# Performance work log

Hardware: AMD Instinct MI355X
Metric: run time of the kernel (lower is better)

## Reference

```python
import jax, jax.numpy as jnp
import numpy as np

NUM_HEADS = 16
HEAD_DIM = 128
NUM_KV_HEADS = 8
NUM_KV_GROUPS = 2
HIDDEN = 2048
SCALE = 0.5  # hardcoded in the original SDPA call


def _fixed_sincos_pos(E, H):
    # matches ReusedProjReconstructor._fixed_sincos_pos (H even here)
    half = H // 2
    freq = jnp.exp(-jnp.log(jnp.float32(10000.0)) * jnp.arange(half, dtype=jnp.float32) / half)
    pos = jnp.arange(E, dtype=jnp.float32)[:, None]
    ang = pos * freq[None, :]
    return jnp.concatenate([jnp.sin(ang), jnp.cos(ang)], axis=1)  # [E, H]


def setup_inputs() -> dict:
    key = jax.random.key(0)
    ks = jax.random.split(key, 8)
    B, M, H = 4, 2048, HIDDEN
    kv_dim = NUM_KV_HEADS * HEAD_DIM
    s = 0.02
    return {
        "mem_act": jax.random.normal(ks[0], (B, M, H), jnp.float32),
        "Wq": jax.random.normal(ks[1], (H, H), jnp.float32) * s,
        "bq": jax.random.normal(ks[2], (H,), jnp.float32) * s,
        "Wk": jax.random.normal(ks[3], (kv_dim, H), jnp.float32) * s,
        "bk": jax.random.normal(ks[4], (kv_dim,), jnp.float32) * s,
        "Wv": jax.random.normal(ks[5], (kv_dim, H), jnp.float32) * s,
        "bv": jax.random.normal(ks[6], (kv_dim,), jnp.float32) * s,
        "Wo": jax.random.normal(ks[7], (H, H), jnp.float32) * s,
        "E": 2048,
    }


def reference(mem_act, Wq, bq, Wk, bk, Wv, bv, Wo, E):
    B, M, H = mem_act.shape
    # positional query hidden, shared across batch (q_ln is Identity)
    q_hidden = _fixed_sincos_pos(E, H).astype(mem_act.dtype)  # [E, H]
    q = (q_hidden @ Wq.T + bq).reshape(E, NUM_HEADS, HEAD_DIM)          # [E, nh, hd]
    k = (mem_act @ Wk.T + bk).reshape(B, M, NUM_KV_HEADS, HEAD_DIM)     # [B, M, nkv, hd]
    v = (mem_act @ Wv.T + bv).reshape(B, M, NUM_KV_HEADS, HEAD_DIM)
    # GQA: repeat kv heads (repeat_interleave over head dim)
    k = jnp.repeat(k, NUM_KV_GROUPS, axis=2)  # [B, M, nh, hd]
    v = jnp.repeat(v, NUM_KV_GROUPS, axis=2)
    # non-causal SDPA with scale=0.5, query broadcast over batch
    scores = jnp.einsum("ehd,bmhd->bhem", q, k) * SCALE  # [B, nh, E, M]
    attn = jax.nn.softmax(scores, axis=-1)
    out = jnp.einsum("bhem,bmhd->behd", attn, v).reshape(B, E, H)
    pred = out @ Wo.T  # o_proj (no bias, Qwen2 style)
    return pred
```

## Files before the change

### kernel.cpp

```cpp
#include <hip/hip_runtime.h>
#include <hip/hip_bf16.h>

typedef __attribute__((ext_vector_type(8))) short short8;
typedef __attribute__((ext_vector_type(4))) float f32x4;
typedef __attribute__((ext_vector_type(16))) float f32x16;
typedef unsigned short ushort_t;

__device__ __forceinline__ unsigned short f2bf(float x) {
    unsigned int u = __builtin_bit_cast(unsigned int, x);
    unsigned int r = (u + 0x7fffu + ((u >> 16) & 1u)) >> 16;
    return (unsigned short)r;
}

__device__ __forceinline__ void gload_lds16(const ushort_t* g, ushort_t* l) {
    __builtin_amdgcn_global_load_lds(
        (const __attribute__((address_space(1))) void*)g,
        (__attribute__((address_space(3))) void*)l, 16, 0, 0);
}

#define MFMA16(A, B, C) __builtin_amdgcn_mfma_f32_16x16x32_bf16((A), (B), (C), 0, 0, 0)
#define MFMA32(A, B, C) __builtin_amdgcn_mfma_f32_32x32x16_bf16((A), (B), (C), 0, 0, 0)

__global__ __launch_bounds__(256) void cvt_f32_bf16(const float* __restrict__ in,
                                                    ushort_t* __restrict__ out, int n) {
    int i = (blockIdx.x * 256 + threadIdx.x) << 3;
    if (i >= n) return;
    const float4* p = (const float4*)(in + i);
    float4 a = p[0], b = p[1];
    short8 o;
    o[0] = (short)f2bf(a.x); o[1] = (short)f2bf(a.y);
    o[2] = (short)f2bf(a.z); o[3] = (short)f2bf(a.w);
    o[4] = (short)f2bf(b.x); o[5] = (short)f2bf(b.y);
    o[6] = (short)f2bf(b.z); o[7] = (short)f2bf(b.w);
    *(short8*)(out + i) = o;
}

__global__ __launch_bounds__(256) void fill_qh(ushort_t* __restrict__ qh) {
    int idx = blockIdx.x * 256 + threadIdx.x;
    int e = idx >> 10, i = idx & 1023;
    float freq = __expf(-9.2103403719761836f * (float)i * (1.0f / 1024.0f));
    float ang = (float)e * freq;
    qh[(size_t)e * 2048 + i]        = f2bf(sinf(ang));
    qh[(size_t)e * 2048 + 1024 + i] = f2bf(cosf(ang));
}

__global__ __launch_bounds__(256) void gemm_q(const ushort_t* __restrict__ A,
                                              const ushort_t* __restrict__ Bw,
                                              const float* __restrict__ bias,
                                              ushort_t* __restrict__ Cout,
                                              int M, int N, int K) {
    __shared__ ushort_t As[128 * 32];
    __shared__ ushort_t Bs[128 * 32];
    const int tid = threadIdx.x;
    const int lane = tid & 63;
    const int wid = tid >> 6;
    const int g = lane >> 4;
    const int r = lane & 15;
    const int wr = wid >> 1, wc = wid & 1;
    const int nbn = N >> 7;
    const int bm = blockIdx.x / nbn, bn = blockIdx.x % nbn;
    const int row0 = bm << 7, col0 = bn << 7;

    f32x4 acc[4][4];
#pragma unroll
    for (int i = 0; i < 4; ++i)
#pragma unroll
        for (int j = 0; j < 4; ++j) acc[i][j] = (f32x4){0.f, 0.f, 0.f, 0.f};

    const int f0 = tid * 8;
    const int r0_ = f0 >> 5, c0_ = f0 & 31;
    const int f1 = (256 + tid) * 8;
    const int r1_ = f1 >> 5, c1_ = f1 & 31;

    for (int k0 = 0; k0 < K; k0 += 32) {
        __syncthreads();
        gload_lds16(A  + (size_t)(row0 + r0_) * K + k0 + c0_, As + f0);
        gload_lds16(A  + (size_t)(row0 + r1_) * K + k0 + c1_, As + f1);
        gload_lds16(Bw + (size_t)(col0 + r0_) * K + k0 + c0_, Bs + f0);
        gload_lds16(Bw + (size_t)(col0 + r1_) * K + k0 + c1_, Bs + f1);
        __syncthreads();
        short8 af[4], bfr[4];
#pragma unroll
        for (int i = 0; i < 4; ++i) {
            af[i]  = *(const short8*)(As + (wr * 64 + i * 16 + r) * 32 + g * 8);
            bfr[i] = *(const short8*)(Bs + (wc * 64 + i * 16 + r) * 32 + g * 8);
        }
#pragma unroll
        for (int i = 0; i < 4; ++i)
#pragma unroll
            for (int j = 0; j < 4; ++j) acc[i][j] = MFMA16(af[i], bfr[j], acc[i][j]);
    }

#pragma unroll
    for (int j = 0; j < 4; ++j) {
        const int col = col0 + wc * 64 + j * 16 + r;
        const float bv = bias[col];
#pragma unroll
        for (int i = 0; i < 4; ++i) {
            const int rowb = row0 + wr * 64 + i * 16 + g * 4;
#pragma unroll
            for (int t = 0; t < 4; ++t) {
                float v = (acc[i][j][t] + bv) * 0.5f;
                Cout[(size_t)(rowb + t) * N + col] = f2bf(v);
            }
        }
    }
}

template <int EPI>
__global__ __launch_bounds__(512, 1) void gemm256(const ushort_t* __restrict__ A,
                                                  const ushort_t* __restrict__ Bw,
                                                  const float* __restrict__ b0,
                                                  const float* __restrict__ b1,
                                                  void* __restrict__ C0,
                                                  void* __restrict__ C1,
                                                  int M, int N, int K) {
    __shared__ ushort_t As[3][256 * 32];
    __shared__ ushort_t Bs[3][256 * 32];
    const int tid = threadIdx.x, lane = tid & 63;
    const int wid = tid >> 6;
    const int q5 = lane & 31, hi = lane >> 5;
    const int wm = wid >> 2, wn = wid & 3;
    const int nbn = N >> 8;
    const int nwg = gridDim.x;
    const int swz = (blockIdx.x & 7) * (nwg >> 3) + (blockIdx.x >> 3);
    const int bm = swz / nbn, bn = swz % nbn;
    const int row0 = bm << 8, col0 = bn << 8;
    const int NT = K >> 5;

    f32x16 acc[4][2];
#pragma unroll
    for (int mi = 0; mi < 4; ++mi)
#pragma unroll
        for (int nj = 0; nj < 2; ++nj)
#pragma unroll
            for (int rr = 0; rr < 16; ++rr) acc[mi][nj][rr] = 0.f;

    auto STAGE = [&](int buf, int kt) {
        const int k0 = kt << 5;
#pragma unroll
        for (int i = 0; i < 2; ++i) {
            const int fb = (i * 512 + tid) << 4;
            const int rp = fb >> 7;
            const int bo = ((fb >> 4) & 7) ^ (rp & 7);
            const int row = rp * 2 + (bo >> 2);
            const int kc = (bo & 3) << 3;
            gload_lds16(A  + (size_t)(row0 + row) * K + k0 + kc, &As[buf][0] + (fb >> 1));
            gload_lds16(Bw + (size_t)(col0 + row) * K + k0 + kc, &Bs[buf][0] + (fb >> 1));
        }
    };

    STAGE(0, 0);
    STAGE(1, 1);
    asm volatile("s_waitcnt vmcnt(4)" ::: "memory");
    __builtin_amdgcn_sched_barrier(0);
    __builtin_amdgcn_s_barrier();
    __builtin_amdgcn_sched_barrier(0);

    for (int t = 0; t < NT; ++t) {
        const int buf = t % 3;
        if (t + 2 < NT) STAGE((t + 2) % 3, t + 2);

        short8 bfr[2][2];
#pragma unroll
        for (int nj = 0; nj < 2; ++nj)
#pragma unroll
            for (int kk = 0; kk < 2; ++kk) {
                const int col = wn * 64 + nj * 32 + q5;
                const int rp = col >> 1;
                const int blk = (((col & 1) << 2) + kk * 2 + hi) ^ (rp & 7);
                bfr[nj][kk] = *(const short8*)((const char*)&Bs[buf][0] + rp * 128 + blk * 16);
            }
#pragma unroll
        for (int mi = 0; mi < 4; ++mi) {
            short8 af[2];
#pragma unroll
            for (int kk = 0; kk < 2; ++kk) {
                const int row = wm * 128 + mi * 32 + q5;
                const int rp = row >> 1;
                const int blk = (((row & 1) << 2) + kk * 2 + hi) ^ (rp & 7);
                af[kk] = *(const short8*)((const char*)&As[buf][0] + rp * 128 + blk * 16);
            }
#pragma unroll
            for (int nj = 0; nj < 2; ++nj) {
                acc[mi][nj] = MFMA32(af[0], bfr[nj][0], acc[mi][nj]);
                acc[mi][nj] = MFMA32(af[1], bfr[nj][1], acc[mi][nj]);
            }
        }

        if (t + 2 < NT) {
            asm volatile("s_waitcnt vmcnt(4)" ::: "memory");
        } else if (t + 1 < NT) {
            asm volatile("s_waitcnt vmcnt(0)" ::: "memory");
        }
        if (t + 1 < NT) {
            __builtin_amdgcn_sched_barrier(0);
            __builtin_amdgcn_s_barrier();
            __builtin_amdgcn_sched_barrier(0);
        }
    }

#pragma unroll
    for (int mi = 0; mi < 4; ++mi)
#pragma unroll
        for (int nj = 0; nj < 2; ++nj) {
            const int col = col0 + wn * 64 + nj * 32 + q5;
            if (EPI == 2) {
                float* outp = (float*)C0;
#pragma unroll
                for (int rr = 0; rr < 16; ++rr) {
                    const int row = row0 + wm * 128 + mi * 32 + (rr & 3) + 8 * (rr >> 2) + 4 * hi;
                    outp[(size_t)row * N + col] = acc[mi][nj][rr];
                }
            } else {
                if (col < 1024) {
                    const float bv = b0[col];
                    ushort_t* Kp = (ushort_t*)C0;
#pragma unroll
                    for (int rr = 0; rr < 16; ++rr) {
                        const int row = row0 + wm * 128 + mi * 32 + (rr & 3) + 8 * (rr >> 2) + 4 * hi;
                        Kp[(size_t)row * 1024 + col] = f2bf(acc[mi][nj][rr] + bv);
                    }
                } else {
                    const int vcol = col - 1024;
                    const float bv = b1[vcol];
                    ushort_t* Vt = (ushort_t*)C1;
#pragma unroll
                    for (int G = 0; G < 4; ++G) {
                        const int m0 = row0 + wm * 128 + mi * 32 + G * 8 + 4 * hi;
                        const int bb = m0 >> 11;
                        const int mm = m0 & 2047;
                        const size_t vtrow = (size_t)(bb * 8 + (vcol >> 7)) * 128 + (vcol & 127);
                        unsigned int p0 = (unsigned int)f2bf(acc[mi][nj][G * 4 + 0] + bv)
                                        | ((unsigned int)f2bf(acc[mi][nj][G * 4 + 1] + bv) << 16);
                        unsigned int p1 = (unsigned int)f2bf(acc[mi][nj][G * 4 + 2] + bv)
                                        | ((unsigned int)f2bf(acc[mi][nj][G * 4 + 3] + bv) << 16);
                        uint2 pk; pk.x = p0; pk.y = p1;
                        *(uint2*)(Vt + vtrow * 2048 + mm) = pk;
                    }
                }
            }
        }
}

__global__ __launch_bounds__(512, 2) void attn_kernel(const ushort_t* __restrict__ Q,
                                                      const ushort_t* __restrict__ Kg,
                                                      const ushort_t* __restrict__ Vt,
                                                      ushort_t* __restrict__ O) {
    __shared__ ushort_t Ks[2][64 * 128];
    __shared__ ushort_t Vts[2][128 * 64];

    const int tid = threadIdx.x, lane = tid & 63, wid = tid >> 6;
    const int q5 = lane & 31;
    const int hi = lane >> 5;
    const int wq = wid & 3;
    const int wg = (blockIdx.x & 7) * 64 + (blockIdx.x >> 3);
    const int bkvh = wg >> 4;
    const int etile = wg & 15;
    const int b = bkvh >> 3, kvh = bkvh & 7;
    const int h = kvh * 2 + (wid >> 2);
    const int e0 = etile * 128;
    const int qrow = e0 + wq * 32 + q5;

    short8 Qf[8];
    {
        const ushort_t* qp = Q + (size_t)qrow * 2048 + h * 128 + hi * 8;
#pragma unroll
        for (int c = 0; c < 8; ++c) Qf[c] = *(const short8*)(qp + c * 16);
    }

    float mrow = -1e30f, lrow = 0.f;
    f32x16 oacc[4];
#pragma unroll
    for (int d0 = 0; d0 < 4; ++d0)
#pragma unroll
        for (int r = 0; r < 16; ++r) oacc[d0][r] = 0.f;

    const ushort_t* Kbase  = Kg + (size_t)b * 2048 * 1024 + kvh * 128;
    const ushort_t* Vtbase = Vt + (size_t)bkvh * 128 * 2048;

    auto STAGE = [&](int buf, int kv0) {
#pragma unroll
        for (int i = 0; i < 2; ++i) {
            const int fb = (i * 8 + wid) * 1024 + lane * 16;
            const int key = fb >> 8;
            const int blk = (fb >> 4) & 15;
            gload_lds16(Kbase + (size_t)(kv0 + key) * 1024 + ((blk ^ (key & 7)) << 3),
                        &Ks[buf][0] + (fb >> 1));
            const int d = fb >> 7;
            const int kb = (fb >> 4) & 7;
            gload_lds16(Vtbase + (size_t)d * 2048 + kv0 + ((kb ^ (d & 7)) << 3),
                        &Vts[buf][0] + (fb >> 1));
        }
    };

    STAGE(0, 0);
    __syncthreads();
    int cur = 0;

    for (int t = 0; t < 32; ++t) {
        if (t < 31) STAGE(cur ^ 1, (t + 1) * 64);
        const char* ks = (const char*)&Ks[cur][0];
        const char* vs = (const char*)&Vts[cur][0];

        f32x16 sS[2];
#pragma unroll
        for (int h2 = 0; h2 < 2; ++h2)
#pragma unroll
            for (int r = 0; r < 16; ++r) sS[h2][r] = 0.f;
#pragma unroll
        for (int h2 = 0; h2 < 2; ++h2) {
            const int key = h2 * 32 + q5;
            const int ksw = key & 7;
#pragma unroll
            for (int c = 0; c < 8; ++c) {
                short8 ka = *(const short8*)(ks + key * 256 + (((c * 2 + hi) ^ ksw) << 4));
                sS[h2] = MFMA32(ka, Qf[c], sS[h2]);
            }
        }

        float vm = fmaxf(sS[0][0], sS[0][1]);
#pragma unroll
        for (int r = 2; r < 16; ++r) vm = fmaxf(vm, sS[0][r]);
#pragma unroll
        for (int r = 0; r < 16; ++r) vm = fmaxf(vm, sS[1][r]);
        vm = fmaxf(vm, __shfl_xor(vm, 32));

        if (__any(vm > mrow + 8.0f)) {
            const float mn = fmaxf(mrow, vm);
            const float esc = __expf(mrow - mn);
            mrow = mn;
            lrow *= esc;
#pragma unroll
            for (int reg = 0; reg < 16; ++reg) {
                const float er = __shfl(esc, (reg & 3) + 8 * (reg >> 2) + 4 * hi);
#pragma unroll
                for (int d0 = 0; d0 < 4; ++d0) oacc[d0][reg] *= er;
            }
        }

        float rs = 0.f;
#pragma unroll
        for (int h2 = 0; h2 < 2; ++h2)
#pragma unroll
            for (int r = 0; r < 16; ++r) {
                const float p = __expf(sS[h2][r] - mrow);
                sS[h2][r] = p;
                rs += p;
            }
        rs += __shfl_xor(rs, 32);
        lrow += rs;

        unsigned int W[2][4][2], Wsw[2][4][2];
#pragma unroll
        for (int h2 = 0; h2 < 2; ++h2)
#pragma unroll
            for (int q4 = 0; q4 < 4; ++q4)
#pragma unroll
                for (int p = 0; p < 2; ++p) {
                    unsigned int w;
                    asm("v_cvt_pk_bf16_f32 %0, %1, %2"
                        : "=v"(w)
                        : "v"(sS[h2][q4 * 4 + 2 * p]), "v"(sS[h2][q4 * 4 + 2 * p + 1]));
                    W[h2][q4][p] = w;
                    Wsw[h2][q4][p] = __shfl_xor(w, 32);
                }

#pragma unroll
        for (int c16 = 0; c16 < 4; ++c16) {
            const int h2 = c16 >> 1;
            const int q4a = (c16 & 1) * 2, q4b = q4a + 1;
            union { unsigned int w[4]; short8 v; } pa;
            pa.w[0] = hi ? Wsw[h2][q4b][0] : W[h2][q4a][0];
            pa.w[1] = hi ? Wsw[h2][q4b][1] : W[h2][q4a][1];
            pa.w[2] = hi ? W[h2][q4b][0] : Wsw[h2][q4a][0];
            pa.w[3] = hi ? W[h2][q4b][1] : Wsw[h2][q4a][1];
#pragma unroll
            for (int d0 = 0; d0 < 4; ++d0) {
                const int d = d0 * 32 + q5;
                short8 vb = *(const short8*)(vs + d * 128 + (((c16 * 2 + hi) ^ (d & 7)) << 4));
                oacc[d0] = MFMA32(pa.v, vb, oacc[d0]);
            }
        }

        __syncthreads();
        cur ^= 1;
    }

#pragma unroll
    for (int reg = 0; reg < 16; ++reg) {
        const int qr = (reg & 3) + 8 * (reg >> 2) + 4 * hi;
        const float lr = __shfl(lrow, qr);
        const float inv = 1.0f / lr;
        const int e = e0 + wq * 32 + qr;
        ushort_t* op = O + ((size_t)b * 2048 + e) * 2048 + h * 128 + q5;
#pragma unroll
        for (int d0 = 0; d0 < 4; ++d0)
            op[d0 * 32] = f2bf(oacc[d0][reg] * inv);
    }
}

extern "C" void kernel_launch(void* const* d_in, const int* in_sizes, int n_in,
                              void* d_out, int out_size, void* d_ws, size_t ws_size,
                              hipStream_t stream) {
    const float* mem_act = (const float*)d_in[0];
    const float* Wq = (const float*)d_in[1];
    const float* bq = (const float*)d_in[2];
    const float* Wk = (const float*)d_in[3];
    const float* bk = (const float*)d_in[4];
    const float* Wv = (const float*)d_in[5];
    const float* bv = (const float*)d_in[6];
    const float* Wo = (const float*)d_in[7];
    float* out = (float*)d_out;

    char* w = (char*)d_ws;
    ushort_t* memb = (ushort_t*)w; w += (size_t)16777216 * 2;
    ushort_t* wqb  = (ushort_t*)w; w += (size_t)4194304 * 2;
    ushort_t* wkvb = (ushort_t*)w; w += (size_t)4194304 * 2;
    ushort_t* wob  = (ushort_t*)w; w += (size_t)4194304 * 2;
    ushort_t* qh   = (ushort_t*)w; w += (size_t)4194304 * 2;
    ushort_t* Qp   = (ushort_t*)w; w += (size_t)4194304 * 2;
    ushort_t* Kp   = (ushort_t*)w; w += (size_t)8388608 * 2;
    ushort_t* Vtp  = (ushort_t*)w; w += (size_t)8388608 * 2;
    ushort_t* AO   = (ushort_t*)w; w += (size_t)16777216 * 2;

    dim3 blk(256);
    cvt_f32_bf16<<<16777216 / 2048, blk, 0, stream>>>(mem_act, memb, 16777216);
    cvt_f32_bf16<<<4194304 / 2048, blk, 0, stream>>>(Wq, wqb, 4194304);
    cvt_f32_bf16<<<2097152 / 2048, blk, 0, stream>>>(Wk, wkvb, 2097152);
    cvt_f32_bf16<<<2097152 / 2048, blk, 0, stream>>>(Wv, wkvb + (size_t)2097152, 2097152);
    cvt_f32_bf16<<<4194304 / 2048, blk, 0, stream>>>(Wo, wob, 4194304);
    fill_qh<<<(2048 * 1024) / 256, blk, 0, stream>>>(qh);

    gemm_q<<<16 * 16, blk, 0, stream>>>(qh, wqb, bq, Qp, 2048, 2048, 2048);

    gemm256<0><<<256, dim3(512), 0, stream>>>(memb, wkvb, bk, bv, Kp, Vtp, 8192, 2048, 2048);

    attn_kernel<<<512, dim3(512), 0, stream>>>(Qp, Kp, Vtp, AO);

    gemm256<2><<<256, dim3(512), 0, stream>>>(AO, wob, nullptr, nullptr, out, nullptr, 8192, 2048, 2048);
}
```

Before: 425.5 us.

## Fuse conversion launches, interleave GEMM staging, use exp2 softmax and MFMA priority

Merges the five fp32-to-bf16 conversion kernels into one launch. Splits the GEMM k-step into two phases, issuing half of the next-stage global-to-LDS loads in each phase and adding an extra barrier between them. Folds log2(e) into the Q scale so the attention softmax can use exp2f instead of expf, with the rescale threshold adjusted to match. Raises wave priority with s_setprio around MFMA blocks in both the GEMM and attention kernels. The extra mid-iteration barrier and the interleaved staging could disturb the existing triple-buffer wait counts.

Measured after the change: 435.3 us. 1.02x slower.

```diff
diff --git a/kernel.cpp b/kernel.cpp
--- a/kernel.cpp
+++ b/kernel.cpp
@@ -21,18 +21,32 @@
 #define MFMA16(A, B, C) __builtin_amdgcn_mfma_f32_16x16x32_bf16((A), (B), (C), 0, 0, 0)
 #define MFMA32(A, B, C) __builtin_amdgcn_mfma_f32_32x32x16_bf16((A), (B), (C), 0, 0, 0)
 
-__global__ __launch_bounds__(256) void cvt_f32_bf16(const float* __restrict__ in,
-                                                    ushort_t* __restrict__ out, int n) {
-    int i = (blockIdx.x * 256 + threadIdx.x) << 3;
-    if (i >= n) return;
-    const float4* p = (const float4*)(in + i);
+__global__ __launch_bounds__(256) void cvt_all(const float* __restrict__ im,
+                                               const float* __restrict__ iq,
+                                               const float* __restrict__ ik,
+                                               const float* __restrict__ iv,
+                                               const float* __restrict__ io,
+                                               ushort_t* __restrict__ om,
+                                               ushort_t* __restrict__ oq,
+                                               ushort_t* __restrict__ ok,
+                                               ushort_t* __restrict__ ov,
+                                               ushort_t* __restrict__ oo) {
+    long i = ((long)blockIdx.x * 256 + threadIdx.x) << 3;
+    const float* s;
+    ushort_t* d;
+    if (i < 16777216)      { s = im + i;              d = om + i; }
+    else if (i < 20971520) { s = iq + (i - 16777216); d = oq + (i - 16777216); }
+    else if (i < 23068672) { s = ik + (i - 20971520); d = ok + (i - 20971520); }
+    else if (i < 25165824) { s = iv + (i - 23068672); d = ov + (i - 23068672); }
+    else                   { s = io + (i - 25165824); d = oo + (i - 25165824); }
+    const float4* p = (const float4*)s;
     float4 a = p[0], b = p[1];
     short8 o;
     o[0] = (short)f2bf(a.x); o[1] = (short)f2bf(a.y);
     o[2] = (short)f2bf(a.z); o[3] = (short)f2bf(a.w);
     o[4] = (short)f2bf(b.x); o[5] = (short)f2bf(b.y);
     o[6] = (short)f2bf(b.z); o[7] = (short)f2bf(b.w);
-    *(short8*)(out + i) = o;
+    *(short8*)d = o;
 }
 
 __global__ __launch_bounds__(256) void fill_qh(ushort_t* __restrict__ qh) {
@@ -100,7 +114,7 @@
             const int rowb = row0 + wr * 64 + i * 16 + g * 4;
 #pragma unroll
             for (int t = 0; t < 4; ++t) {
-                float v = (acc[i][j][t] + bv) * 0.5f;
+                float v = (acc[i][j][t] + bv) * 0.7213475204444817f;
                 Cout[(size_t)(rowb + t) * N + col] = f2bf(v);
             }
         }
@@ -136,22 +150,19 @@
 #pragma unroll
             for (int rr = 0; rr < 16; ++rr) acc[mi][nj][rr] = 0.f;
 
-    auto STAGE = [&](int buf, int kt) {
+    auto STAGE_HALF = [&](int buf, int kt, int i) {
         const int k0 = kt << 5;
-#pragma unroll
-        for (int i = 0; i < 2; ++i) {
-            const int fb = (i * 512 + tid) << 4;
-            const int rp = fb >> 7;
-            const int bo = ((fb >> 4) & 7) ^ (rp & 7);
-            const int row = rp * 2 + (bo >> 2);
-            const int kc = (bo & 3) << 3;
-            gload_lds16(A  + (size_t)(row0 + row) * K + k0 + kc, &As[buf][0] + (fb >> 1));
-            gload_lds16(Bw + (size_t)(col0 + row) * K + k0 + kc, &Bs[buf][0] + (fb >> 1));
-        }
+        const int fb = (i * 512 + tid) << 4;
+        const int rp = fb >> 7;
+        const int bo = ((fb >> 4) & 7) ^ (rp & 7);
+        const int row = rp * 2 + (bo >> 2);
+        const int kc = (bo & 3) << 3;
+        gload_lds16(A  + (size_t)(row0 + row) * K + k0 + kc, &As[buf][0] + (fb >> 1));
+        gload_lds16(Bw + (size_t)(col0 + row) * K + k0 + kc, &Bs[buf][0] + (fb >> 1));
     };
 
-    STAGE(0, 0);
-    STAGE(1, 1);
+    STAGE_HALF(0, 0, 0); STAGE_HALF(0, 0, 1);
+    STAGE_HALF(1, 1, 0); STAGE_HALF(1, 1, 1);
     asm volatile("s_waitcnt vmcnt(4)" ::: "memory");
     __builtin_amdgcn_sched_barrier(0);
     __builtin_amdgcn_s_barrier();
@@ -159,32 +170,37 @@
 
     for (int t = 0; t < NT; ++t) {
         const int buf = t % 3;
-        if (t + 2 < NT) STAGE((t + 2) % 3, t + 2);
-
-        short8 bfr[2][2];
-#pragma unroll
-        for (int nj = 0; nj < 2; ++nj)
-#pragma unroll
-            for (int kk = 0; kk < 2; ++kk) {
+        const char* Ab = (const char*)&As[buf][0];
+        const char* Bb = (const char*)&Bs[buf][0];
+#pragma unroll
+        for (int ph = 0; ph < 2; ++ph) {
+            short8 af[4], bfr[2];
+#pragma unroll
+            for (int nj = 0; nj < 2; ++nj) {
                 const int col = wn * 64 + nj * 32 + q5;
                 const int rp = col >> 1;
-                const int blk = (((col & 1) << 2) + kk * 2 + hi) ^ (rp & 7);
-                bfr[nj][kk] = *(const short8*)((const char*)&Bs[buf][0] + rp * 128 + blk * 16);
-            }
-#pragma unroll
-        for (int mi = 0; mi < 4; ++mi) {
-            short8 af[2];
-#pragma unroll
-            for (int kk = 0; kk < 2; ++kk) {
+                const int blk = (((col & 1) << 2) + ph * 2 + hi) ^ (rp & 7);
+                bfr[nj] = *(const short8*)(Bb + rp * 128 + blk * 16);
+            }
+#pragma unroll
+            for (int mi = 0; mi < 4; ++mi) {
                 const int row = wm * 128 + mi * 32 + q5;
                 const int rp = row >> 1;
-                const int blk = (((row & 1) << 2) + kk * 2 + hi) ^ (rp & 7);
-                af[kk] = *(const short8*)((const char*)&As[buf][0] + rp * 128 + blk * 16);
-            }
-#pragma unroll
-            for (int nj = 0; nj < 2; ++nj) {
-                acc[mi][nj] = MFMA32(af[0], bfr[nj][0], acc[mi][nj]);
-                acc[mi][nj] = MFMA32(af[1], bfr[nj][1], acc[mi][nj]);
+                const int blk = (((row & 1) << 2) + ph * 2 + hi) ^ (rp & 7);
+                af[mi] = *(const short8*)(Ab + rp * 128 + blk * 16);
+            }
+            if (t + 2 < NT) STAGE_HALF((t + 2) % 3, t + 2, ph);
+            __builtin_amdgcn_s_setprio(1);
+#pragma unroll
+            for (int mi = 0; mi < 4; ++mi)
+#pragma unroll
+                for (int nj = 0; nj < 2; ++nj)
+                    acc[mi][nj] = MFMA32(af[mi], bfr[nj], acc[mi][nj]);
+            __builtin_amdgcn_s_setprio(0);
+            if (ph == 0) {
+                __builtin_amdgcn_sched_barrier(0);
+                __builtin_amdgcn_s_barrier();
+                __builtin_amdgcn_sched_barrier(0);
             }
         }
 
@@ -308,6 +324,7 @@
         for (int h2 = 0; h2 < 2; ++h2)
 #pragma unroll
             for (int r = 0; r < 16; ++r) sS[h2][r] = 0.f;
+        __builtin_amdgcn_s_setprio(1);
 #pragma unroll
         for (int h2 = 0; h2 < 2; ++h2) {
             const int key = h2 * 32 + q5;
@@ -318,6 +335,7 @@
                 sS[h2] = MFMA32(ka, Qf[c], sS[h2]);
             }
         }
+        __builtin_amdgcn_s_setprio(0);
 
         float vm = fmaxf(sS[0][0], sS[0][1]);
 #pragma unroll
@@ -326,9 +344,9 @@
         for (int r = 0; r < 16; ++r) vm = fmaxf(vm, sS[1][r]);
         vm = fmaxf(vm, __shfl_xor(vm, 32));
 
-        if (__any(vm > mrow + 8.0f)) {
+        if (__any(vm > mrow + 11.54f)) {
             const float mn = fmaxf(mrow, vm);
-            const float esc = __expf(mrow - mn);
+            const float esc = exp2f(mrow - mn);
             mrow = mn;
             lrow *= esc;
 #pragma unroll
@@ -344,7 +362,7 @@
         for (int h2 = 0; h2 < 2; ++h2)
 #pragma unroll
             for (int r = 0; r < 16; ++r) {
-                const float p = __expf(sS[h2][r] - mrow);
+                const float p = exp2f(sS[h2][r] - mrow);
                 sS[h2][r] = p;
                 rs += p;
             }
@@ -375,12 +393,14 @@
             pa.w[1] = hi ? Wsw[h2][q4b][1] : W[h2][q4a][1];
             pa.w[2] = hi ? W[h2][q4b][0] : Wsw[h2][q4a][0];
             pa.w[3] = hi ? W[h2][q4b][1] : Wsw[h2][q4a][1];
+            __builtin_amdgcn_s_setprio(1);
 #pragma unroll
             for (int d0 = 0; d0 < 4; ++d0) {
                 const int d = d0 * 32 + q5;
                 short8 vb = *(const short8*)(vs + d * 128 + (((c16 * 2 + hi) ^ (d & 7)) << 4));
                 oacc[d0] = MFMA32(pa.v, vb, oacc[d0]);
             }
+            __builtin_amdgcn_s_setprio(0);
         }
 
         __syncthreads();
@@ -425,11 +445,8 @@
     ushort_t* AO   = (ushort_t*)w; w += (size_t)16777216 * 2;
 
     dim3 blk(256);
-    cvt_f32_bf16<<<16777216 / 2048, blk, 0, stream>>>(mem_act, memb, 16777216);
-    cvt_f32_bf16<<<4194304 / 2048, blk, 0, stream>>>(Wq, wqb, 4194304);
-    cvt_f32_bf16<<<2097152 / 2048, blk, 0, stream>>>(Wk, wkvb, 2097152);
-    cvt_f32_bf16<<<2097152 / 2048, blk, 0, stream>>>(Wv, wkvb + (size_t)2097152, 2097152);
-    cvt_f32_bf16<<<4194304 / 2048, blk, 0, stream>>>(Wo, wob, 4194304);
+    cvt_all<<<14336, blk, 0, stream>>>(mem_act, Wq, Wk, Wv, Wo,
+                                       memb, wqb, wkvb, wkvb + (size_t)2097152, wob);
     fill_qh<<<(2048 * 1024) / 256, blk, 0, stream>>>(qh);
 
     gemm_q<<<16 * 16, blk, 0, stream>>>(qh, wqb, bq, Qp, 2048, 2048, 2048);
```
